# Optimization experiments

Measured on AMD Instinct MI355X. Metric: run time of the kernel, lower is better.

Reference implementation:

```python
import math
import jax, jax.numpy as jnp
import numpy as np
from jax.scipy.special import xlogy, gammaln

HEADS = 8
DIM_KEY = 64
NUM_REL_POS_FEATURES = 192


def get_positional_embed(n, feature_size):
    # distances: [-n+1, ..., n-1], length 2n-1
    dist = jnp.arange(-n + 1, n)
    adist = jnp.abs(dist).astype(jnp.float32)[:, None]  # (2n-1, 1)
    num_basis = feature_size // 6  # 3 feature fns * 2 (sign-augmented)
    seq_len = n
    # exponential half-life features
    max_range = math.log(seq_len) / math.log(2.0)
    half_life = 2.0 ** jnp.linspace(3.0, max_range, num_basis)  # min_half_life=3.0
    feat_exp = jnp.exp(-math.log(2.0) / half_life[None, :] * adist)
    # central mask features
    center_widths = 2.0 ** jnp.arange(1, num_basis + 1) - 1.0
    feat_cm = (center_widths[None, :] > adist).astype(jnp.float32)
    # gamma pdf features
    stddev = seq_len / (2 * num_basis)
    start_mean = seq_len / num_basis
    mean = jnp.linspace(start_mean, float(seq_len), num_basis)[None, :]
    concentration = (mean / stddev) ** 2
    rate = mean / (stddev ** 2)
    log_unnorm = xlogy(concentration - 1.0, adist) - rate * adist
    log_norm = gammaln(concentration) - concentration * jnp.log(rate)
    prob = jnp.exp(log_unnorm - log_norm) + 1e-8
    feat_gamma = prob / jnp.max(prob, axis=-1, keepdims=True)
    emb = jnp.concatenate([feat_exp, feat_cm, feat_gamma], axis=-1)  # (2n-1, fs/2)
    sign = jnp.sign(dist).astype(jnp.float32)[:, None]
    return jnp.concatenate([emb, sign * emb], axis=-1)  # (2n-1, fs)


def relative_shift(x):
    # x: (b, h, n, 2n-1) -> (b, h, n, n) Transformer-XL shift
    b, h, t1, t2 = x.shape
    x = jnp.pad(x, ((0, 0), (0, 0), (0, 0), (1, 0)))  # (b,h,t1,t2+1)
    x = x.reshape(b, h, t2 + 1, t1)[:, :, 1:, :].reshape(b, h, t1, t2)
    return x[..., : (t2 + 2) // 2]


def setup_inputs() -> dict:
    key = jax.random.key(0)
    ks = jax.random.split(key, 8)
    dim = 1536
    b, n = 2, 1536
    hdk = HEADS * DIM_KEY  # 512
    hdv = HEADS * 192      # 1536
    s = 0.02
    return {
        'x': jax.random.normal(ks[0], (b, n, dim), jnp.float32),
        'Wq': jax.random.normal(ks[1], (hdk, dim), jnp.float32) * s,
        'Wk': jax.random.normal(ks[2], (hdk, dim), jnp.float32) * s,
        'Wv': jax.random.normal(ks[3], (hdv, dim), jnp.float32) * s,
        'Wrel': jax.random.normal(ks[4], (hdk, NUM_REL_POS_FEATURES), jnp.float32) * s,
        'Wout': jax.random.normal(ks[5], (dim, hdv), jnp.float32) * s,
        'b_out': jnp.zeros((dim,), jnp.float32),
        'rel_content_bias': jax.random.normal(ks[6], (1, HEADS, 1, DIM_KEY), jnp.float32),
        'rel_pos_bias': jax.random.normal(ks[7], (1, HEADS, 1, DIM_KEY), jnp.float32),
    }


def reference(x, Wq, Wk, Wv, Wrel, Wout, b_out, rel_content_bias, rel_pos_bias):
    b, n, dim = x.shape
    h = HEADS
    scale = DIM_KEY ** -0.5

    def split_heads(t):  # (b, n, h*d) -> (b, h, n, d)
        return t.reshape(b, n, h, -1).transpose(0, 2, 1, 3)

    q = split_heads(jnp.einsum('bnd,fd->bnf', x, Wq)) * scale
    k = split_heads(jnp.einsum('bnd,fd->bnf', x, Wk))
    v = split_heads(jnp.einsum('bnd,fd->bnf', x, Wv))

    content_logits = jnp.einsum('bhid,bhjd->bhij', q + rel_content_bias, k)

    positions = get_positional_embed(n, NUM_REL_POS_FEATURES)  # (2n-1, fs)
    rel_k = jnp.einsum('jf,ef->je', positions, Wrel).reshape(2 * n - 1, h, DIM_KEY)
    rel_k = rel_k.transpose(1, 0, 2)  # (h, 2n-1, dk)
    rel_logits = jnp.einsum('bhid,hjd->bhij', q + rel_pos_bias, rel_k)
    rel_logits = relative_shift(rel_logits)  # (b, h, n, n)

    attn = jax.nn.softmax(content_logits + rel_logits, axis=-1)
    out = jnp.einsum('bhij,bhjd->bhid', attn, v)
    out = out.transpose(0, 2, 1, 3).reshape(b, n, -1)  # (b, n, h*dv)
    return jnp.einsum('bnf,df->bnd', out, Wout) + b_out
```

## Files before the change

kernel.cpp:

```cpp
#include <hip/hip_runtime.h>
#include <cmath>

typedef unsigned short u16;
typedef unsigned int u32;
typedef short frag8 __attribute__((ext_vector_type(8)));
typedef float f32x4 __attribute__((ext_vector_type(4)));

#define DEVINL __device__ __forceinline__

DEVINL float bf2f(u16 v) { return __uint_as_float(((u32)v) << 16); }
DEVINL u16 f2bf(float f) {
    u32 u = __float_as_uint(f);
    u32 r = (u + 0x7fffu + ((u >> 16) & 1u)) >> 16;
    return (u16)r;
}
DEVINL u32 pack2(float a, float b) { return (u32)f2bf(a) | ((u32)f2bf(b) << 16); }
DEVINL void async_copy16(const u16* g, u16* l) {
    __builtin_amdgcn_global_load_lds((const __attribute__((address_space(1))) u32*)g,
                                     (__attribute__((address_space(3))) u32*)l, 16, 0, 0);
}
DEVINL f32x4 mfma_bf16(frag8 a, frag8 b, f32x4 c) {
    return __builtin_amdgcn_mfma_f32_16x16x32_bf16(a, b, c, 0, 0, 0);
}

__global__ __launch_bounds__(256) void convert_kernel(
        const float* __restrict__ s0, const float* __restrict__ s1,
        const float* __restrict__ s2, const float* __restrict__ s3,
        const float* __restrict__ s4, u16* __restrict__ dst) {
    const int c0 = 589824, c1 = 98304, c2 = 98304, c3 = 294912;
    const int total = 1376256;
    for (int c = blockIdx.x * blockDim.x + threadIdx.x; c < total;
         c += gridDim.x * blockDim.x) {
        const float* src; int off;
        if (c < c0) { src = s0; off = c; }
        else if (c < c0 + c1) { src = s1; off = c - c0; }
        else if (c < c0 + c1 + c2) { src = s2; off = c - c0 - c1; }
        else if (c < c0 + c1 + c2 + c3) { src = s3; off = c - c0 - c1 - c2; }
        else { src = s4; off = c - c0 - c1 - c2 - c3; }
        float4 a = ((const float4*)src)[off * 2];
        float4 b = ((const float4*)src)[off * 2 + 1];
        uint4 o;
        o.x = pack2(a.x, a.y); o.y = pack2(a.z, a.w);
        o.z = pack2(b.x, b.y); o.w = pack2(b.z, b.w);
        ((uint4*)dst)[c] = o;
    }
}

DEVINL double lgamma_stirling(double z) {
    double zi = 1.0 / z, zi2 = zi * zi;
    return (z - 0.5) * log(z) - z + 0.91893853320467274178
         + zi * (1.0 / 12.0) - zi * zi2 * (1.0 / 360.0) + zi * zi2 * zi2 * (1.0 / 1260.0);
}

__global__ __launch_bounds__(256) void embed_relk_kernel(const float* __restrict__ Wrel,
                                                         u16* __restrict__ relk) {
    __shared__ float pos[16][192];
    __shared__ float inv_hl[32], cwid[32], cm1[32], rateS[32];
    __shared__ double lognS[32];
    __shared__ float gmax[16];
    int t = threadIdx.x;
    int u0b = blockIdx.x * 16;

    if (t < 32) {
        double step = (10.584962500721156 - 3.0) / 31.0;
        double hl = exp2(3.0 + t * step);
        inv_hl[t] = (float)(1.0 / hl);
        cwid[t] = exp2f((float)(t + 1)) - 1.0f;
        double mean = 48.0 * (t + 1);
        double conc = (mean / 24.0) * (mean / 24.0);
        double rate = mean / 576.0;
        cm1[t] = (float)(conc - 1.0);
        rateS[t] = (float)rate;
        lognS[t] = lgamma_stirling(conc) - conc * log(rate);
    }
    __syncthreads();

    for (int idx = t; idx < 512; idx += 256) {
        int ul = idx >> 5, bs = idx & 31;
        int dist = u0b + ul - 1535;
        float ad = fabsf((float)dist);
        pos[ul][bs] = exp2f(-ad * inv_hl[bs]);
        pos[ul][32 + bs] = (cwid[bs] > ad) ? 1.0f : 0.0f;
        double prob = 0.0;
        if (dist != 0) {
            double adD = (double)ad;
            prob = exp((double)cm1[bs] * log(adD) - (double)rateS[bs] * adD - lognS[bs]);
        }
        pos[ul][64 + bs] = (float)(prob + 1e-8);
    }
    __syncthreads();
    if (t < 16) {
        float g = 0.f;
        #pragma unroll
        for (int bsx = 0; bsx < 32; bsx++) g = fmaxf(g, pos[t][64 + bsx]);
        gmax[t] = g;
    }
    __syncthreads();
    for (int idx = t; idx < 16 * 96; idx += 256) {
        int ul = idx / 96, f = idx - ul * 96;
        float v = pos[ul][f];
        if (f >= 64) { v = v / gmax[ul]; pos[ul][f] = v; }
        int dist = u0b + ul - 1535;
        float sg = (dist > 0) ? 1.f : ((dist < 0) ? -1.f : 0.f);
        pos[ul][96 + f] = sg * v;
    }
    __syncthreads();

    int e0 = t * 2;
    const float* w0 = Wrel + e0 * 192;
    const float* w1 = w0 + 192;
    float a0[16], a1[16];
    #pragma unroll
    for (int ul = 0; ul < 16; ul++) { a0[ul] = 0.f; a1[ul] = 0.f; }
    for (int f = 0; f < 192; f++) {
        float wa = w0[f], wb = w1[f];
        #pragma unroll
        for (int ul = 0; ul < 16; ul++) {
            float p = pos[ul][f];
            a0[ul] = fmaf(p, wa, a0[ul]);
            a1[ul] = fmaf(p, wb, a1[ul]);
        }
    }
    int h0 = e0 >> 6, d0 = e0 & 63;
    int h1 = (e0 + 1) >> 6, d1 = (e0 + 1) & 63;
    for (int ul = 0; ul < 16; ul++) {
        int u = u0b + ul;
        relk[(h0 * 3072 + u) * 64 + d0] = f2bf(a0[ul]);
        relk[(h1 * 3072 + u) * 64 + d1] = f2bf(a1[ul]);
    }
}

DEVINL void gemm128_mainloop(const u16* __restrict__ A, const u16* __restrict__ B,
                             int K, f32x4 acc[4][4], u16* As, u16* Bs) {
    int tid = threadIdx.x;
    int lane = tid & 63, wave = tid >> 6;
    int wm = (wave >> 1) * 64, wn = (wave & 1) * 64;
    int fm = lane & 15, fq = lane >> 4;
    for (int k0 = 0; k0 < K; k0 += 32) {
        #pragma unroll
        for (int p = 0; p < 2; p++) {
            int e = (p * 256 + tid) * 8;
            int r = e >> 5, c = e & 31;
            async_copy16(A + r * K + k0 + c, As + e);
            async_copy16(B + r * K + k0 + c, Bs + e);
        }
        __syncthreads();
        frag8 af[4], bfr[4];
        #pragma unroll
        for (int mi = 0; mi < 4; mi++) af[mi] = *(const frag8*)&As[(wm + 16 * mi + fm) * 32 + fq * 8];
        #pragma unroll
        for (int ni = 0; ni < 4; ni++) bfr[ni] = *(const frag8*)&Bs[(wn + 16 * ni + fm) * 32 + fq * 8];
        #pragma unroll
        for (int mi = 0; mi < 4; mi++)
            #pragma unroll
            for (int ni = 0; ni < 4; ni++)
                acc[mi][ni] = mfma_bf16(af[mi], bfr[ni], acc[mi][ni]);
        __syncthreads();
    }
}

__global__ __launch_bounds__(256) void gemm_qkv_kernel(
        const u16* __restrict__ X, const u16* __restrict__ Wq, const u16* __restrict__ Wk,
        const u16* __restrict__ Wv, const float* __restrict__ cbias, const float* __restrict__ pbias,
        u16* __restrict__ qc, u16* __restrict__ qp, u16* __restrict__ kws, u16* __restrict__ vt) {
    __shared__ __align__(16) u16 As[128 * 32];
    __shared__ __align__(16) u16 Bs[128 * 32];
    int m0 = blockIdx.x * 128, n0 = blockIdx.y * 128;
    const u16* Bp; int brow;
    if (n0 < 512)       { Bp = Wq; brow = n0; }
    else if (n0 < 1024) { Bp = Wk; brow = n0 - 512; }
    else                { Bp = Wv; brow = n0 - 1024; }
    f32x4 acc[4][4];
    #pragma unroll
    for (int i = 0; i < 4; i++)
        #pragma unroll
        for (int j = 0; j < 4; j++) acc[i][j] = (f32x4){0.f, 0.f, 0.f, 0.f};
    gemm128_mainloop(X + m0 * 1536, Bp + brow * 1536, 1536, acc, As, Bs);

    int tid = threadIdx.x, lane = tid & 63, wave = tid >> 6;
    int wm = (wave >> 1) * 64, wn = (wave & 1) * 64, fm = lane & 15, fq = lane >> 4;
    #pragma unroll
    for (int mi = 0; mi < 4; mi++) {
        #pragma unroll
        for (int ni = 0; ni < 4; ni++) {
            int col = n0 + wn + 16 * ni + fm;
            int rbase = m0 + wm + 16 * mi + fq * 4;
            #pragma unroll
            for (int reg = 0; reg < 4; reg++) {
                int row = rbase + reg;
                float v = acc[mi][ni][reg];
                int b = row >= 1536 ? 1 : 0;
                int i = row - b * 1536;
                if (n0 < 512) {
                    float qv = v * 0.125f;
                    int idx = ((b * 8 + (col >> 6)) * 1536 + i) * 64 + (col & 63);
                    qc[idx] = f2bf(qv + cbias[col]);
                    qp[idx] = f2bf(qv + pbias[col]);
                } else if (n0 < 1024) {
                    int c2 = col - 512;
                    kws[((b * 8 + (c2 >> 6)) * 1536 + i) * 64 + (c2 & 63)] = f2bf(v);
                } else {
                    int c2 = col - 1024;
                    int hh = c2 / 192, dd = c2 - hh * 192;
                    vt[((b * 8 + hh) * 192 + dd) * 1536 + i] = f2bf(v);
                }
            }
        }
    }
}

__global__ __launch_bounds__(256) void attn_kernel(
        const u16* __restrict__ qc, const u16* __restrict__ qp, const u16* __restrict__ kws,
        const u16* __restrict__ vt, const u16* __restrict__ relk, u16* __restrict__ ao) {
    __shared__ __align__(16) u16 smem[24768];
    u16* k_lds    = smem;
    u16* vt_lds   = smem + 4096;
    u16* relk_lds = smem + 16384;
    u16* P_lds    = smem + 22528;
    float* S_lds  = (float*)k_lds;
    float* R_lds  = (float*)relk_lds;
    float* mstate = (float*)(smem + 24576);
    float* lstate = mstate + 32;
    float* alpha_lds = lstate + 32;

    const int n = 1536;
    int bh = blockIdx.y, b = bh >> 3, h = bh & 7;
    int i0 = blockIdx.x * 32;
    const u16* qcP = qc + bh * n * 64;
    const u16* qpP = qp + bh * n * 64;
    const u16* kP  = kws + bh * n * 64;
    const u16* vtP = vt + bh * 192 * n;
    const u16* rkP = relk + h * 3072 * 64;

    int tid = threadIdx.x, lane = tid & 63, w = tid >> 6, fm = lane & 15, fq = lane >> 4;
    int sw = fm & 7;
    if (tid < 32) { mstate[tid] = __int_as_float(0xff800000); lstate[tid] = 0.f; }

    frag8 aqc[2][2], aqp[2][2];
    #pragma unroll
    for (int mi = 0; mi < 2; mi++)
        #pragma unroll
        for (int ks = 0; ks < 2; ks++) {
            int off = (i0 + 16 * mi + fm) * 64 + ks * 32 + fq * 8;
            aqc[mi][ks] = *(const frag8*)(qcP + off);
            aqp[mi][ks] = *(const frag8*)(qpP + off);
        }

    f32x4 acc_o[2][3];
    #pragma unroll
    for (int mi = 0; mi < 2; mi++)
        #pragma unroll
        for (int dj = 0; dj < 3; dj++) acc_o[mi][dj] = (f32x4){0.f, 0.f, 0.f, 0.f};

    int uis[3], rmis[3];
    #pragma unroll
    for (int tt = 0; tt < 3; tt++) {
        int tv = w + tt * 4;
        rmis[tt] = (tv >= 6) ? 1 : 0;
        uis[tt] = tv - rmis[tt] * 6;
    }

    for (int jt = 0; jt < 24; jt++) {
        int j0 = jt * 64;
        __syncthreads();
        #pragma unroll
        for (int p = 0; p < 2; p++) {
            int l = p * 256 + tid, r = l >> 3, c = (l & 7) ^ (r & 7);
            async_copy16(kP + (j0 + r) * 64 + c * 8, k_lds + l * 8);
        }
        #pragma unroll
        for (int p = 0; p < 6; p++) {
            int l = p * 256 + tid, r = l >> 3, c = (l & 7) ^ (r & 7);
            async_copy16(vtP + r * n + j0 + c * 8, vt_lds + l * 8);
        }
        int u0 = 1504 + j0 - i0;
        #pragma unroll
        for (int p = 0; p < 3; p++) {
            int l = p * 256 + tid, r = l >> 3, c = (l & 7) ^ (r & 7);
            async_copy16(rkP + (u0 + r) * 64 + c * 8, relk_lds + l * 8);
        }
        __syncthreads();

        f32x4 acc_s[2];
        acc_s[0] = (f32x4){0.f, 0.f, 0.f, 0.f};
        acc_s[1] = (f32x4){0.f, 0.f, 0.f, 0.f};
        #pragma unroll
        for (int ks = 0; ks < 2; ks++) {
            frag8 bk = *(const frag8*)&k_lds[(16 * w + fm) * 64 + ((ks * 4 + fq) ^ sw) * 8];
            acc_s[0] = mfma_bf16(aqc[0][ks], bk, acc_s[0]);
            acc_s[1] = mfma_bf16(aqc[1][ks], bk, acc_s[1]);
        }
        f32x4 acc_r[3];
        #pragma unroll
        for (int tt = 0; tt < 3; tt++) {
            acc_r[tt] = (f32x4){0.f, 0.f, 0.f, 0.f};
            #pragma unroll
            for (int ks = 0; ks < 2; ks++) {
                frag8 br = *(const frag8*)&relk_lds[(16 * uis[tt] + fm) * 64 + ((ks * 4 + fq) ^ sw) * 8];
                acc_r[tt] = mfma_bf16(aqp[rmis[tt]][ks], br, acc_r[tt]);
            }
        }
        __syncthreads();

        #pragma unroll
        for (int mi = 0; mi < 2; mi++)
            #pragma unroll
            for (int reg = 0; reg < 4; reg++)
                S_lds[(16 * mi + fq * 4 + reg) * 64 + 16 * w + fm] = acc_s[mi][reg];
        #pragma unroll
        for (int tt = 0; tt < 3; tt++)
            #pragma unroll
            for (int reg = 0; reg < 4; reg++)
                R_lds[(16 * rmis[tt] + fq * 4 + reg) * 96 + 16 * uis[tt] + fm] = acc_r[tt][reg];
        __syncthreads();

        int li = tid >> 3, c0 = (tid & 7) * 8;
        float sv[8];
        float mx = __int_as_float(0xff800000);
        #pragma unroll
        for (int e = 0; e < 8; e++) {
            int c = c0 + e;
            sv[e] = S_lds[li * 64 + c] + R_lds[li * 96 + c - li + 31];
            mx = fmaxf(mx, sv[e]);
        }
        mx = fmaxf(mx, __shfl_xor(mx, 1));
        mx = fmaxf(mx, __shfl_xor(mx, 2));
        mx = fmaxf(mx, __shfl_xor(mx, 4));
        float mo = mstate[li];
        float mn = fmaxf(mo, mx);
        float al = __expf(mo - mn);
        float pe[8], sum = 0.f;
        #pragma unroll
        for (int e = 0; e < 8; e++) { pe[e] = __expf(sv[e] - mn); sum += pe[e]; }
        {
            uint4 pw;
            pw.x = pack2(pe[0], pe[1]); pw.y = pack2(pe[2], pe[3]);
            pw.z = pack2(pe[4], pe[5]); pw.w = pack2(pe[6], pe[7]);
            int slot = (tid & 7) ^ (li & 7);
            *(uint4*)&P_lds[li * 64 + slot * 8] = pw;
        }
        sum += __shfl_xor(sum, 1);
        sum += __shfl_xor(sum, 2);
        sum += __shfl_xor(sum, 4);
        if ((tid & 7) == 0) {
            mstate[li] = mn;
            lstate[li] = lstate[li] * al + sum;
            alpha_lds[li] = al;
        }
        __syncthreads();

        #pragma unroll
        for (int mi = 0; mi < 2; mi++)
            #pragma unroll
            for (int reg = 0; reg < 4; reg++) {
                float al2 = alpha_lds[16 * mi + fq * 4 + reg];
                #pragma unroll
                for (int dj = 0; dj < 3; dj++) acc_o[mi][dj][reg] *= al2;
            }
        frag8 ap[2][2];
        #pragma unroll
        for (int mi = 0; mi < 2; mi++)
            #pragma unroll
            for (int ks = 0; ks < 2; ks++)
                ap[mi][ks] = *(const frag8*)&P_lds[(16 * mi + fm) * 64 + ((ks * 4 + fq) ^ sw) * 8];
        #pragma unroll
        for (int dj = 0; dj < 3; dj++) {
            #pragma unroll
            for (int ks = 0; ks < 2; ks++) {
                frag8 bv = *(const frag8*)&vt_lds[(16 * (3 * w + dj) + fm) * 64 + ((ks * 4 + fq) ^ sw) * 8];
                acc_o[0][dj] = mfma_bf16(ap[0][ks], bv, acc_o[0][dj]);
                acc_o[1][dj] = mfma_bf16(ap[1][ks], bv, acc_o[1][dj]);
            }
        }
    }

    __syncthreads();
    #pragma unroll
    for (int mi = 0; mi < 2; mi++)
        #pragma unroll
        for (int dj = 0; dj < 3; dj++)
            #pragma unroll
            for (int reg = 0; reg < 4; reg++) {
                int rl = 16 * mi + fq * 4 + reg;
                float lsum = lstate[rl];
                int row = b * 1536 + i0 + rl;
                int col = h * 192 + 16 * (3 * w + dj) + fm;
                ao[row * 1536 + col] = f2bf(acc_o[mi][dj][reg] / lsum);
            }
}

__global__ __launch_bounds__(256) void gemm_out_kernel(
        const u16* __restrict__ A, const u16* __restrict__ W, const float* __restrict__ bias,
        float* __restrict__ out) {
    __shared__ __align__(16) u16 As[128 * 32];
    __shared__ __align__(16) u16 Bs[128 * 32];
    int m0 = blockIdx.x * 128, n0 = blockIdx.y * 128;
    f32x4 acc[4][4];
    #pragma unroll
    for (int i = 0; i < 4; i++)
        #pragma unroll
        for (int j = 0; j < 4; j++) acc[i][j] = (f32x4){0.f, 0.f, 0.f, 0.f};
    gemm128_mainloop(A + m0 * 1536, W + n0 * 1536, 1536, acc, As, Bs);

    int tid = threadIdx.x, lane = tid & 63, wave = tid >> 6;
    int wm = (wave >> 1) * 64, wn = (wave & 1) * 64, fm = lane & 15, fq = lane >> 4;
    #pragma unroll
    for (int mi = 0; mi < 4; mi++) {
        #pragma unroll
        for (int ni = 0; ni < 4; ni++) {
            int col = n0 + wn + 16 * ni + fm;
            int rbase = m0 + wm + 16 * mi + fq * 4;
            float bv = bias[col];
            #pragma unroll
            for (int reg = 0; reg < 4; reg++) {
                int row = rbase + reg;
                out[row * 1536 + col] = acc[mi][ni][reg] + bv;
            }
        }
    }
}

extern "C" void kernel_launch(void* const* d_in, const int* in_sizes, int n_in,
                              void* d_out, int out_size, void* d_ws, size_t ws_size,
                              hipStream_t stream) {
    (void)in_sizes; (void)n_in; (void)out_size; (void)ws_size;
    const float* x    = (const float*)d_in[0];
    const float* Wq   = (const float*)d_in[1];
    const float* Wk   = (const float*)d_in[2];
    const float* Wv   = (const float*)d_in[3];
    const float* Wrel = (const float*)d_in[4];
    const float* Wout = (const float*)d_in[5];
    const float* bout = (const float*)d_in[6];
    const float* cb   = (const float*)d_in[7];
    const float* pb   = (const float*)d_in[8];

    u16* xb  = (u16*)d_ws;
    u16* wqb = xb  + 4718592;
    u16* wkb = wqb + 786432;
    u16* wvb = wkb + 786432;
    u16* wob = wvb + 2359296;
    u16* qc  = wob + 2359296;
    u16* qp  = qc + 1572864;
    u16* kw  = qp + 1572864;
    u16* vt  = kw + 1572864;
    u16* rk  = vt + 4718592;
    u16* ao  = rk + 1572864;
    float* out = (float*)d_out;

    convert_kernel<<<dim3(1024), dim3(256), 0, stream>>>(x, Wq, Wk, Wv, Wout, xb);
    embed_relk_kernel<<<dim3(192), dim3(256), 0, stream>>>(Wrel, rk);
    gemm_qkv_kernel<<<dim3(24, 20), dim3(256), 0, stream>>>(xb, wqb, wkb, wvb, cb, pb, qc, qp, kw, vt);
    attn_kernel<<<dim3(48, 16), dim3(256), 0, stream>>>(qc, qp, kw, vt, rk, ao);
    gemm_out_kernel<<<dim3(24, 12), dim3(256), 0, stream>>>(ao, wob, bout, out);
}
```

Baseline: 327.2 us.

## Load K, V and rel-K fragments directly from global memory instead of via LDS

Removes the per-tile async global-to-LDS staging of K, V^T and relative-key tiles, along with two barriers per iteration. Each wave now reads its MFMA B-fragments straight from global memory through pointer iterators. The S and R score buffers get padded strides to reduce LDS bank conflicts, and S is read with float4 loads. With the smaller LDS footprint, launch bounds now request four blocks per CU. The cost is that MFMA operands become global loads, which rely on L1/L2 caching and lose the explicit prefetch.

```diff
diff --git a/kernel.cpp b/kernel.cpp
--- a/kernel.cpp
+++ b/kernel.cpp
@@ -209,28 +209,22 @@
     }
 }
 
-__global__ __launch_bounds__(256) void attn_kernel(
+#define SP 68
+#define RP 100
+
+__global__ __launch_bounds__(256, 4) void attn_kernel(
         const u16* __restrict__ qc, const u16* __restrict__ qp, const u16* __restrict__ kws,
         const u16* __restrict__ vt, const u16* __restrict__ relk, u16* __restrict__ ao) {
-    __shared__ __align__(16) u16 smem[24768];
-    u16* k_lds    = smem;
-    u16* vt_lds   = smem + 4096;
-    u16* relk_lds = smem + 16384;
-    u16* P_lds    = smem + 22528;
-    float* S_lds  = (float*)k_lds;
-    float* R_lds  = (float*)relk_lds;
-    float* mstate = (float*)(smem + 24576);
-    float* lstate = mstate + 32;
-    float* alpha_lds = lstate + 32;
+    __shared__ __align__(16) float S_lds[32 * SP];
+    __shared__ __align__(16) float R_lds[32 * RP];
+    __shared__ __align__(16) u16 P_lds[32 * 64];
+    __shared__ float mstate[32], lstate[32], alpha_lds[32];
 
     const int n = 1536;
     int bh = blockIdx.y, b = bh >> 3, h = bh & 7;
     int i0 = blockIdx.x * 32;
     const u16* qcP = qc + bh * n * 64;
     const u16* qpP = qp + bh * n * 64;
-    const u16* kP  = kws + bh * n * 64;
-    const u16* vtP = vt + bh * 192 * n;
-    const u16* rkP = relk + h * 3072 * 64;
 
     int tid = threadIdx.x, lane = tid & 63, w = tid >> 6, fm = lane & 15, fq = lane >> 4;
     int sw = fm & 7;
@@ -260,33 +254,17 @@
         uis[tt] = tv - rmis[tt] * 6;
     }
 
+    const u16* kIt  = kws + bh * n * 64 + (16 * w + fm) * 64 + fq * 8;
+    const u16* vIt  = vt + bh * 192 * n + (48 * w + fm) * 1536 + fq * 8;
+    const u16* rkIt = relk + h * 3072 * 64 + (1504 - i0 + fm) * 64 + fq * 8;
+
     for (int jt = 0; jt < 24; jt++) {
-        int j0 = jt * 64;
-        __syncthreads();
-        #pragma unroll
-        for (int p = 0; p < 2; p++) {
-            int l = p * 256 + tid, r = l >> 3, c = (l & 7) ^ (r & 7);
-            async_copy16(kP + (j0 + r) * 64 + c * 8, k_lds + l * 8);
-        }
-        #pragma unroll
-        for (int p = 0; p < 6; p++) {
-            int l = p * 256 + tid, r = l >> 3, c = (l & 7) ^ (r & 7);
-            async_copy16(vtP + r * n + j0 + c * 8, vt_lds + l * 8);
-        }
-        int u0 = 1504 + j0 - i0;
-        #pragma unroll
-        for (int p = 0; p < 3; p++) {
-            int l = p * 256 + tid, r = l >> 3, c = (l & 7) ^ (r & 7);
-            async_copy16(rkP + (u0 + r) * 64 + c * 8, relk_lds + l * 8);
-        }
-        __syncthreads();
-
         f32x4 acc_s[2];
         acc_s[0] = (f32x4){0.f, 0.f, 0.f, 0.f};
         acc_s[1] = (f32x4){0.f, 0.f, 0.f, 0.f};
         #pragma unroll
         for (int ks = 0; ks < 2; ks++) {
-            frag8 bk = *(const frag8*)&k_lds[(16 * w + fm) * 64 + ((ks * 4 + fq) ^ sw) * 8];
+            frag8 bk = *(const frag8*)(kIt + ks * 32);
             acc_s[0] = mfma_bf16(aqc[0][ks], bk, acc_s[0]);
             acc_s[1] = mfma_bf16(aqc[1][ks], bk, acc_s[1]);
         }
@@ -294,9 +272,10 @@
         #pragma unroll
         for (int tt = 0; tt < 3; tt++) {
             acc_r[tt] = (f32x4){0.f, 0.f, 0.f, 0.f};
+            const u16* rp = rkIt + uis[tt] * 1024;
             #pragma unroll
             for (int ks = 0; ks < 2; ks++) {
-                frag8 br = *(const frag8*)&relk_lds[(16 * uis[tt] + fm) * 64 + ((ks * 4 + fq) ^ sw) * 8];
+                frag8 br = *(const frag8*)(rp + ks * 32);
                 acc_r[tt] = mfma_bf16(aqp[rmis[tt]][ks], br, acc_r[tt]);
             }
         }
@@ -306,21 +285,27 @@
         for (int mi = 0; mi < 2; mi++)
             #pragma unroll
             for (int reg = 0; reg < 4; reg++)
-                S_lds[(16 * mi + fq * 4 + reg) * 64 + 16 * w + fm] = acc_s[mi][reg];
+                S_lds[(16 * mi + fq * 4 + reg) * SP + 16 * w + fm] = acc_s[mi][reg];
         #pragma unroll
         for (int tt = 0; tt < 3; tt++)
             #pragma unroll
             for (int reg = 0; reg < 4; reg++)
-                R_lds[(16 * rmis[tt] + fq * 4 + reg) * 96 + 16 * uis[tt] + fm] = acc_r[tt][reg];
+                R_lds[(16 * rmis[tt] + fq * 4 + reg) * RP + 16 * uis[tt] + fm] = acc_r[tt][reg];
         __syncthreads();
 
         int li = tid >> 3, c0 = (tid & 7) * 8;
         float sv[8];
+        {
+            float4 sa = *(const float4*)(S_lds + li * SP + c0);
+            float4 sb = *(const float4*)(S_lds + li * SP + c0 + 4);
+            sv[0] = sa.x; sv[1] = sa.y; sv[2] = sa.z; sv[3] = sa.w;
+            sv[4] = sb.x; sv[5] = sb.y; sv[6] = sb.z; sv[7] = sb.w;
+        }
+        const float* rrow = R_lds + li * RP + c0 - li + 31;
         float mx = __int_as_float(0xff800000);
         #pragma unroll
         for (int e = 0; e < 8; e++) {
-            int c = c0 + e;
-            sv[e] = S_lds[li * 64 + c] + R_lds[li * 96 + c - li + 31];
+            sv[e] += rrow[e];
             mx = fmaxf(mx, sv[e]);
         }
         mx = fmaxf(mx, __shfl_xor(mx, 1));
@@ -365,16 +350,20 @@
                 ap[mi][ks] = *(const frag8*)&P_lds[(16 * mi + fm) * 64 + ((ks * 4 + fq) ^ sw) * 8];
         #pragma unroll
         for (int dj = 0; dj < 3; dj++) {
+            const u16* vp = vIt + dj * 24576;
             #pragma unroll
             for (int ks = 0; ks < 2; ks++) {
-                frag8 bv = *(const frag8*)&vt_lds[(16 * (3 * w + dj) + fm) * 64 + ((ks * 4 + fq) ^ sw) * 8];
+                frag8 bv = *(const frag8*)(vp + ks * 32);
                 acc_o[0][dj] = mfma_bf16(ap[0][ks], bv, acc_o[0][dj]);
                 acc_o[1][dj] = mfma_bf16(ap[1][ks], bv, acc_o[1][dj]);
             }
         }
-    }
-
-    __syncthreads();
+
+        kIt += 64 * 64;
+        vIt += 64;
+        rkIt += 64 * 64;
+    }
+
     #pragma unroll
     for (int mi = 0; mi < 2; mi++)
         #pragma unroll
```

Result: slower. 346.9 us (+6.0%).
